# Performance work log

Measured on AMD Instinct MI355X. Metric: run time of the kernel, lower is better.

Reference implementation:

```python
import jax, jax.numpy as jnp
import numpy as np

N_NODES = 50000
N_EDGES = 400000
MUL_IN = 32      # input node irreps: 32x0e
MUL_OUT = 64     # target irreps: 64x0e+64x1o+64x2e+64x3o
DENOM = 8.0

# component-normalized real spherical harmonics, l = 1, 2, 3, on unit vectors
_S3, _S5, _S7, _S15, _S42, _S70, _S105 = (np.sqrt(v).astype(np.float32) for v in (3., 5., 7., 15., 42., 70., 105.))

def spherical_harmonics_123(vec):
    # vec: [E, 3]; normalize=True semantics
    r = jnp.linalg.norm(vec, axis=-1, keepdims=True)
    u = vec / jnp.maximum(r, 1e-12)
    x, y, z = u[..., 0], u[..., 1], u[..., 2]
    x2, y2, z2 = x * x, y * y, z * z
    sh1 = jnp.stack([_S3 * x, _S3 * y, _S3 * z], axis=-1)                      # [E, 3]
    sh2 = jnp.stack([
        _S15 * x * y,
        _S15 * y * z,
        0.5 * _S5 * (3.0 * z2 - 1.0),
        _S15 * x * z,
        0.5 * _S15 * (x2 - y2),
    ], axis=-1)                                                                # [E, 5]
    sh3 = jnp.stack([
        0.25 * _S70 * y * (3.0 * x2 - y2),
        _S105 * x * y * z,
        0.25 * _S42 * y * (5.0 * z2 - 1.0),
        0.5 * _S7 * z * (5.0 * z2 - 3.0),
        0.25 * _S42 * x * (5.0 * z2 - 1.0),
        0.5 * _S105 * z * (x2 - y2),
        0.25 * _S70 * x * (x2 - 3.0 * y2),
    ], axis=-1)                                                                # [E, 7]
    return sh1, sh2, sh3


def setup_inputs() -> dict:
    key = jax.random.key(0)
    ks = jax.random.split(key, 9)
    return {
        "positions": jax.random.normal(ks[0], (N_NODES, 3), jnp.float32),
        "node_feats": jax.random.normal(ks[1], (N_NODES, MUL_IN), jnp.float32),
        "W0": jax.random.normal(ks[2], (MUL_IN, MUL_OUT), jnp.float32),
        "W1": jax.random.normal(ks[3], (MUL_IN, MUL_OUT), jnp.float32),
        "W2": jax.random.normal(ks[4], (MUL_IN, MUL_OUT), jnp.float32),
        "W3": jax.random.normal(ks[5], (MUL_IN, MUL_OUT), jnp.float32),
        "Wsc": jax.random.normal(ks[6], (MUL_IN, MUL_OUT), jnp.float32),
        "senders": jax.random.randint(ks[7], (N_EDGES,), 0, N_NODES),
        "receivers": jax.random.randint(ks[8], (N_EDGES,), 0, N_NODES),
    }


def reference(positions, node_feats, W0, W1, W2, W3, Wsc, senders, receivers):
    E = senders.shape[0]
    # ---- update_edge_fn: gather senders, SH of edge vectors, 0e x l tensor product ----
    sf = node_feats[senders]                                      # [E, 32] (32x0e)
    rel = positions[receivers] - positions[senders]               # [E, 3]
    sh1, sh2, sh3 = spherical_harmonics_123(rel)
    # tensor product 32x0e (x) (1o+2e+3o): CG for 0e x l -> l is identity
    tp1 = (sf[:, :, None] * sh1[:, None, :]).reshape(E, -1)       # [E, 32*3]
    tp2 = (sf[:, :, None] * sh2[:, None, :]).reshape(E, -1)       # [E, 32*5]
    tp3 = (sf[:, :, None] * sh3[:, None, :]).reshape(E, -1)       # [E, 32*7]
    messages = jnp.concatenate([sf, tp1, tp2, tp3], axis=-1)      # [E, 512]: 32x0e+32x1o+32x2e+32x3o

    # ---- GraphNetwork aggregation: sum messages at receivers ----
    agg = jax.ops.segment_sum(messages, receivers, num_segments=N_NODES)  # [N, 512]
    nf = agg / DENOM

    # ---- update_node_fn: e3nn Linear per-l (path-normalized by 1/sqrt(fan_in)) ----
    scale = 1.0 / np.sqrt(MUL_IN).astype(np.float32)
    s = nf[:, :MUL_IN]                                            # [N, 32]
    v1 = nf[:, MUL_IN:MUL_IN * 4].reshape(-1, MUL_IN, 3)
    v2 = nf[:, MUL_IN * 4:MUL_IN * 9].reshape(-1, MUL_IN, 5)
    v3 = nf[:, MUL_IN * 9:].reshape(-1, MUL_IN, 7)

    out0 = (s @ W0) * scale                                       # [N, 64]
    out1 = jnp.einsum('nmi,mt->nti', v1, W1) * scale              # [N, 64, 3]
    out2 = jnp.einsum('nmi,mt->nti', v2, W2) * scale              # [N, 64, 5]
    out3 = jnp.einsum('nmi,mt->nti', v3, W3) * scale              # [N, 64, 7]

    # shortcut Linear from 32x0e (force_irreps_out: only the 0e block is nonzero)
    out0 = out0 + (node_feats @ Wsc) * scale

    N = node_feats.shape[0]
    return jnp.concatenate(
        [out0, out1.reshape(N, -1), out2.reshape(N, -1), out3.reshape(N, -1)], axis=-1
    )  # [N, 1024]
```

## Files before the change

### kernel.cpp

```cpp
#include <hip/hip_runtime.h>

#define NN 50000
#define NE 400000
#define SCAN_NB 196

__global__ void k_hist(const int* __restrict__ rcv, int* __restrict__ cnt){
  int e = blockIdx.x*256 + threadIdx.x;
  if (e < NE) atomicAdd(&cnt[rcv[e]], 1);
}

__global__ void k_scanA(const int* __restrict__ cnt, int* __restrict__ bsum){
  __shared__ int sh[256];
  int i = blockIdx.x*256 + threadIdx.x;
  int v = (i < NN) ? cnt[i] : 0;
  sh[threadIdx.x] = v; __syncthreads();
  for (int off=128; off>0; off>>=1){
    if (threadIdx.x < off) sh[threadIdx.x] += sh[threadIdx.x+off];
    __syncthreads();
  }
  if (threadIdx.x==0) bsum[blockIdx.x] = sh[0];
}

__global__ void k_scanB(int* __restrict__ bsum){
  __shared__ int sh[256];
  int t = threadIdx.x;
  int v = (t < SCAN_NB) ? bsum[t] : 0;
  sh[t] = v; __syncthreads();
  for (int off=1; off<256; off<<=1){
    int x = (t>=off)? sh[t-off] : 0;
    __syncthreads();
    sh[t] += x;
    __syncthreads();
  }
  if (t < SCAN_NB) bsum[t] = sh[t] - v;
}

__global__ void k_scanC(const int* __restrict__ cnt, const int* __restrict__ bsum,
                        int* __restrict__ offs, int* __restrict__ cursor){
  __shared__ int sh[256];
  int t = threadIdx.x;
  int i = blockIdx.x*256 + t;
  int v = (i < NN) ? cnt[i] : 0;
  sh[t] = v; __syncthreads();
  for (int off=1; off<256; off<<=1){
    int x = (t>=off)? sh[t-off] : 0;
    __syncthreads();
    sh[t] += x;
    __syncthreads();
  }
  int excl = sh[t] - v + bsum[blockIdx.x];
  if (i < NN){ offs[i] = excl; cursor[i] = excl; }
}

__global__ void k_scatter(const int* __restrict__ rcv, const int* __restrict__ snd,
                          int* __restrict__ cursor, int* __restrict__ csr_snd){
  int e = blockIdx.x*256 + threadIdx.x;
  if (e < NE){
    int p = atomicAdd(&cursor[rcv[e]], 1);
    csr_snd[p] = snd[e];
  }
}

__global__ void k_prepW(const float* __restrict__ W0, const float* __restrict__ W1,
                        const float* __restrict__ W2, const float* __restrict__ W3,
                        float4* __restrict__ Wp){
  int i = blockIdx.x*256 + threadIdx.x;
  if (i < 2048) Wp[i] = make_float4(W0[i], W1[i], W2[i], W3[i]);
}

__global__ __launch_bounds__(256) void k_main(
    const float* __restrict__ pos, const float* __restrict__ feat,
    const float4* __restrict__ Wp, const float* __restrict__ Wsc,
    const int* __restrict__ offs, const int* __restrict__ cnt,
    const int* __restrict__ csr_snd, float* __restrict__ out)
{
  __shared__ __align__(16) float smS[4][1024];

  const int tid = threadIdx.x, wv = tid>>6, lane = tid&63;
  const int ml = lane&31, hh = lane>>5;
  const int n = blockIdx.x*4 + wv;
  const float pnx=pos[n*3], pny=pos[n*3+1], pnz=pos[n*3+2];
  const int start = offs[n], deg = cnt[n];
  const int nch = (deg+63)>>6;

  float acc[8];
  #pragma unroll
  for (int j=0;j<8;++j) acc[j]=0.f;

  const float SC3=1.7320508f, SC5=2.236068f, SC7=2.6457513f, SC15=3.8729833f,
              SC42=6.4807407f, SC70=8.3666003f, SC105=10.246951f;

  for (int c=0; c<nch; ++c){
    const int base = c<<6;
    int cn = deg - base; cn = (cn>64)?64:cn;
    int sE = 0;
    if (lane < cn){
      sE = csr_snd[start+base+lane];
      float rx = pnx - pos[sE*3];
      float ry = pny - pos[sE*3+1];
      float rz = pnz - pos[sE*3+2];
      float r = sqrtf(rx*rx+ry*ry+rz*rz);
      float inv = 1.0f/fmaxf(r,1e-12f);
      float x=rx*inv, y=ry*inv, z=rz*inv;
      float x2=x*x, y2=y*y, z2=z*z;
      float s1=SC3*x, s2=SC3*y, s3=SC3*z;
      float s4=SC15*x*y, s5=SC15*y*z, s6=0.5f*SC5*(3.f*z2-1.f), s7=SC15*x*z;
      float s8=0.5f*SC15*(x2-y2);
      float s9 =0.25f*SC70*y*(3.f*x2-y2);
      float s10=SC105*x*y*z;
      float s11=0.25f*SC42*y*(5.f*z2-1.f);
      float s12=0.5f*SC7*z*(5.f*z2-3.f);
      float s13=0.25f*SC42*x*(5.f*z2-1.f);
      float s14=0.5f*SC105*z*(x2-y2);
      float s15=0.25f*SC70*x*(x2-3.f*y2);
      float4* wp = (float4*)&smS[wv][lane*16];
      wp[0] = make_float4(1.0f,s1,s2,s3);
      wp[1] = make_float4(s4,s5,s6,s7);
      wp[2] = make_float4(s8,s9,s10,s11);
      wp[3] = make_float4(s12,s13,s14,s15);
    }
    asm volatile("s_waitcnt lgkmcnt(0)" ::: "memory");
    #pragma unroll 8
    for (int it=0; it<cn; ++it){
      int s = __builtin_amdgcn_readlane(sE, it);
      float f = feat[(size_t)s*32 + ml];
      const float4* rp = (const float4*)&smS[wv][it*16 + hh*8];
      float4 q0=rp[0], q1=rp[1];
      acc[0]+=f*q0.x; acc[1]+=f*q0.y; acc[2]+=f*q0.z; acc[3]+=f*q0.w;
      acc[4]+=f*q1.x; acc[5]+=f*q1.y; acc[6]+=f*q1.z; acc[7]+=f*q1.w;
    }
    asm volatile("" ::: "memory");
  }

  {
    float4* ap = (float4*)&smS[wv][ml*16 + hh*8];
    ap[0] = make_float4(acc[0],acc[1],acc[2],acc[3]);
    ap[1] = make_float4(acc[4],acc[5],acc[6],acc[7]);
  }
  asm volatile("s_waitcnt lgkmcnt(0)" ::: "memory");

  float oa[16];
  #pragma unroll
  for (int k=0;k<16;++k) oa[k]=0.f;
  float osc = 0.f;
  const float4* f4 = (const float4*)(feat + (size_t)n*32);

  #pragma unroll 2
  for (int g=0; g<8; ++g){
    float4 fsv = f4[g];
    #pragma unroll
    for (int mm=0; mm<4; ++mm){
      const int m = g*4+mm;
      float4 wq = Wp[m*64 + lane];
      float  w4 = Wsc[m*64 + lane];
      const float4* Ap = (const float4*)&smS[wv][m*16];
      float4 a0=Ap[0], a1=Ap[1], a2=Ap[2], a3=Ap[3];
      const float fsm = (mm==0)?fsv.x:(mm==1)?fsv.y:(mm==2)?fsv.z:fsv.w;
      oa[0] += a0.x*wq.x;
      oa[1] += a0.y*wq.y; oa[2] += a0.z*wq.y; oa[3] += a0.w*wq.y;
      oa[4] += a1.x*wq.z; oa[5] += a1.y*wq.z; oa[6] += a1.z*wq.z;
      oa[7] += a1.w*wq.z; oa[8] += a2.x*wq.z;
      oa[9] += a2.y*wq.w; oa[10]+= a2.z*wq.w; oa[11]+= a2.w*wq.w;
      oa[12]+= a3.x*wq.w; oa[13]+= a3.y*wq.w; oa[14]+= a3.z*wq.w; oa[15]+= a3.w*wq.w;
      osc += fsm*w4;
    }
  }
  asm volatile("" ::: "memory");

  const float S = 0.17677669529663687f;
  const float S8 = S*0.125f;
  float* ol = &smS[wv][0];
  ol[lane] = oa[0]*S8 + osc*S;
  #pragma unroll
  for (int i=0;i<3;++i) ol[64  + lane*3 + i] = oa[1+i]*S8;
  #pragma unroll
  for (int i=0;i<5;++i) ol[256 + lane*5 + i] = oa[4+i]*S8;
  #pragma unroll
  for (int i=0;i<7;++i) ol[576 + lane*7 + i] = oa[9+i]*S8;
  asm volatile("s_waitcnt lgkmcnt(0)" ::: "memory");

  float4* o4 = (float4*)(out + (size_t)n*1024);
  const float4* s4 = (const float4*)&smS[wv][0];
  #pragma unroll
  for (int i=0;i<4;++i) o4[i*64 + lane] = s4[i*64 + lane];
}

extern "C" void kernel_launch(void* const* d_in, const int* in_sizes, int n_in,
                              void* d_out, int out_size, void* d_ws, size_t ws_size,
                              hipStream_t stream) {
  const float* pos  = (const float*)d_in[0];
  const float* feat = (const float*)d_in[1];
  const float* W0   = (const float*)d_in[2];
  const float* W1   = (const float*)d_in[3];
  const float* W2   = (const float*)d_in[4];
  const float* W3   = (const float*)d_in[5];
  const float* Wsc  = (const float*)d_in[6];
  const int*  snd   = (const int*)d_in[7];
  const int*  rcv   = (const int*)d_in[8];
  float* out = (float*)d_out;

  int* ws      = (int*)d_ws;
  int* cnt     = ws;
  int* offs    = ws + 50000;
  int* cursor  = ws + 100000;
  int* bsum    = ws + 150000;
  int* csr_snd = ws + 150272;
  float4* Wp   = (float4*)(ws + 550272);

  hipMemsetAsync(cnt, 0, NN*sizeof(int), stream);
  k_hist   <<<(NE+255)/256, 256, 0, stream>>>(rcv, cnt);
  k_scanA  <<<SCAN_NB, 256, 0, stream>>>(cnt, bsum);
  k_scanB  <<<1, 256, 0, stream>>>(bsum);
  k_scanC  <<<SCAN_NB, 256, 0, stream>>>(cnt, bsum, offs, cursor);
  k_scatter<<<(NE+255)/256, 256, 0, stream>>>(rcv, snd, cursor, csr_snd);
  k_prepW  <<<8, 256, 0, stream>>>(W0, W1, W2, W3, Wp);
  k_main   <<<12500, 256, 0, stream>>>(pos, feat, Wp, Wsc,
                                       offs, cnt, csr_snd, out);
}
```

Baseline: 396.3 us.

## Process two nodes per wavefront and broadcast aggregates via readlane

```diff
diff --git a/kernel.cpp b/kernel.cpp
--- a/kernel.cpp
+++ b/kernel.cpp
@@ -74,115 +74,123 @@
     const int* __restrict__ offs, const int* __restrict__ cnt,
     const int* __restrict__ csr_snd, float* __restrict__ out)
 {
-  __shared__ __align__(16) float smS[4][1024];
+  __shared__ __align__(16) float smS[4][1280];
 
   const int tid = threadIdx.x, wv = tid>>6, lane = tid&63;
   const int ml = lane&31, hh = lane>>5;
-  const int n = blockIdx.x*4 + wv;
-  const float pnx=pos[n*3], pny=pos[n*3+1], pnz=pos[n*3+2];
-  const int start = offs[n], deg = cnt[n];
-  const int nch = (deg+63)>>6;
-
-  float acc[8];
-  #pragma unroll
-  for (int j=0;j<8;++j) acc[j]=0.f;
+  const int nb = blockIdx.x*8 + wv*2;
 
   const float SC3=1.7320508f, SC5=2.236068f, SC7=2.6457513f, SC15=3.8729833f,
               SC42=6.4807407f, SC70=8.3666003f, SC105=10.246951f;
 
-  for (int c=0; c<nch; ++c){
-    const int base = c<<6;
-    int cn = deg - base; cn = (cn>64)?64:cn;
-    int sE = 0;
-    if (lane < cn){
-      sE = csr_snd[start+base+lane];
-      float rx = pnx - pos[sE*3];
-      float ry = pny - pos[sE*3+1];
-      float rz = pnz - pos[sE*3+2];
-      float r = sqrtf(rx*rx+ry*ry+rz*rz);
-      float inv = 1.0f/fmaxf(r,1e-12f);
-      float x=rx*inv, y=ry*inv, z=rz*inv;
-      float x2=x*x, y2=y*y, z2=z*z;
-      float s1=SC3*x, s2=SC3*y, s3=SC3*z;
-      float s4=SC15*x*y, s5=SC15*y*z, s6=0.5f*SC5*(3.f*z2-1.f), s7=SC15*x*z;
-      float s8=0.5f*SC15*(x2-y2);
-      float s9 =0.25f*SC70*y*(3.f*x2-y2);
-      float s10=SC105*x*y*z;
-      float s11=0.25f*SC42*y*(5.f*z2-1.f);
-      float s12=0.5f*SC7*z*(5.f*z2-3.f);
-      float s13=0.25f*SC42*x*(5.f*z2-1.f);
-      float s14=0.5f*SC105*z*(x2-y2);
-      float s15=0.25f*SC70*x*(x2-3.f*y2);
-      float4* wp = (float4*)&smS[wv][lane*16];
-      wp[0] = make_float4(1.0f,s1,s2,s3);
-      wp[1] = make_float4(s4,s5,s6,s7);
-      wp[2] = make_float4(s8,s9,s10,s11);
-      wp[3] = make_float4(s12,s13,s14,s15);
+  float acc[2][8];
+  #pragma unroll
+  for (int nn=0;nn<2;++nn)
+    #pragma unroll
+    for (int j=0;j<8;++j) acc[nn][j]=0.f;
+
+  #pragma unroll
+  for (int nn=0; nn<2; ++nn){
+    const int n = nb + nn;
+    const float pnx=pos[n*3], pny=pos[n*3+1], pnz=pos[n*3+2];
+    const int start = offs[n], deg = cnt[n];
+    const int nch = (deg+63)>>6;
+    for (int c=0; c<nch; ++c){
+      const int base = c<<6;
+      int cn = deg - base; cn = (cn>64)?64:cn;
+      int sE = 0;
+      if (lane < cn){
+        sE = csr_snd[start+base+lane];
+        float rx = pnx - pos[sE*3];
+        float ry = pny - pos[sE*3+1];
+        float rz = pnz - pos[sE*3+2];
+        float r = sqrtf(rx*rx+ry*ry+rz*rz);
+        float inv = 1.0f/fmaxf(r,1e-12f);
+        float x=rx*inv, y=ry*inv, z=rz*inv;
+        float x2=x*x, y2=y*y, z2=z*z;
+        float s1=SC3*x, s2=SC3*y, s3=SC3*z;
+        float s4=SC15*x*y, s5=SC15*y*z, s6=0.5f*SC5*(3.f*z2-1.f), s7=SC15*x*z;
+        float s8=0.5f*SC15*(x2-y2);
+        float s9 =0.25f*SC70*y*(3.f*x2-y2);
+        float s10=SC105*x*y*z;
+        float s11=0.25f*SC42*y*(5.f*z2-1.f);
+        float s12=0.5f*SC7*z*(5.f*z2-3.f);
+        float s13=0.25f*SC42*x*(5.f*z2-1.f);
+        float s14=0.5f*SC105*z*(x2-y2);
+        float s15=0.25f*SC70*x*(x2-3.f*y2);
+        float4* wp = (float4*)&smS[wv][lane*20];
+        wp[0] = make_float4(1.0f,s1,s2,s3);
+        wp[1] = make_float4(s4,s5,s6,s7);
+        wp[2] = make_float4(s8,s9,s10,s11);
+        wp[3] = make_float4(s12,s13,s14,s15);
+      }
+      asm volatile("s_waitcnt lgkmcnt(0)" ::: "memory");
+      #pragma unroll 8
+      for (int it=0; it<cn; ++it){
+        int s = __builtin_amdgcn_readlane(sE, it);
+        float f = feat[(size_t)s*32 + ml];
+        const float4* rp = (const float4*)&smS[wv][it*20 + hh*8];
+        float4 q0=rp[0], q1=rp[1];
+        acc[nn][0]+=f*q0.x; acc[nn][1]+=f*q0.y;
+        acc[nn][2]+=f*q0.z; acc[nn][3]+=f*q0.w;
+        acc[nn][4]+=f*q1.x; acc[nn][5]+=f*q1.y;
+        acc[nn][6]+=f*q1.z; acc[nn][7]+=f*q1.w;
+      }
+      asm volatile("" ::: "memory");
     }
-    asm volatile("s_waitcnt lgkmcnt(0)" ::: "memory");
-    #pragma unroll 8
-    for (int it=0; it<cn; ++it){
-      int s = __builtin_amdgcn_readlane(sE, it);
-      float f = feat[(size_t)s*32 + ml];
-      const float4* rp = (const float4*)&smS[wv][it*16 + hh*8];
-      float4 q0=rp[0], q1=rp[1];
-      acc[0]+=f*q0.x; acc[1]+=f*q0.y; acc[2]+=f*q0.z; acc[3]+=f*q0.w;
-      acc[4]+=f*q1.x; acc[5]+=f*q1.y; acc[6]+=f*q1.z; acc[7]+=f*q1.w;
+  }
+
+  const int n0 = __builtin_amdgcn_readfirstlane(nb);
+  const float* fn0 = feat + (size_t)n0*32;
+  const float* fn1 = fn0 + 32;
+
+  float oa[2][16];
+  #pragma unroll
+  for (int nn=0;nn<2;++nn)
+    #pragma unroll
+    for (int k=0;k<16;++k) oa[nn][k]=0.f;
+  float osc0=0.f, osc1=0.f;
+
+  #pragma unroll 4
+  for (int m=0; m<32; ++m){
+    float4 wq = Wp[m*64 + lane];
+    float  w4 = Wsc[m*64 + lane];
+    float f0 = fn0[m], f1 = fn1[m];
+    osc0 += f0*w4; osc1 += f1*w4;
+    #pragma unroll
+    for (int k=0;k<16;++k){
+      const int src = m + ((k>>3)<<5);
+      float a0 = __int_as_float(__builtin_amdgcn_readlane(
+                   __float_as_int(acc[0][k&7]), src));
+      float a1 = __int_as_float(__builtin_amdgcn_readlane(
+                   __float_as_int(acc[1][k&7]), src));
+      const float w = (k==0)?wq.x : (k<4)?wq.y : (k<9)?wq.z : wq.w;
+      oa[0][k] += a0*w;
+      oa[1][k] += a1*w;
     }
-    asm volatile("" ::: "memory");
-  }
-
-  {
-    float4* ap = (float4*)&smS[wv][ml*16 + hh*8];
-    ap[0] = make_float4(acc[0],acc[1],acc[2],acc[3]);
-    ap[1] = make_float4(acc[4],acc[5],acc[6],acc[7]);
-  }
-  asm volatile("s_waitcnt lgkmcnt(0)" ::: "memory");
-
-  float oa[16];
-  #pragma unroll
-  for (int k=0;k<16;++k) oa[k]=0.f;
-  float osc = 0.f;
-  const float4* f4 = (const float4*)(feat + (size_t)n*32);
-
-  #pragma unroll 2
-  for (int g=0; g<8; ++g){
-    float4 fsv = f4[g];
-    #pragma unroll
-    for (int mm=0; mm<4; ++mm){
-      const int m = g*4+mm;
-      float4 wq = Wp[m*64 + lane];
-      float  w4 = Wsc[m*64 + lane];
-      const float4* Ap = (const float4*)&smS[wv][m*16];
-      float4 a0=Ap[0], a1=Ap[1], a2=Ap[2], a3=Ap[3];
-      const float fsm = (mm==0)?fsv.x:(mm==1)?fsv.y:(mm==2)?fsv.z:fsv.w;
-      oa[0] += a0.x*wq.x;
-      oa[1] += a0.y*wq.y; oa[2] += a0.z*wq.y; oa[3] += a0.w*wq.y;
-      oa[4] += a1.x*wq.z; oa[5] += a1.y*wq.z; oa[6] += a1.z*wq.z;
-      oa[7] += a1.w*wq.z; oa[8] += a2.x*wq.z;
-      oa[9] += a2.y*wq.w; oa[10]+= a2.z*wq.w; oa[11]+= a2.w*wq.w;
-      oa[12]+= a3.x*wq.w; oa[13]+= a3.y*wq.w; oa[14]+= a3.z*wq.w; oa[15]+= a3.w*wq.w;
-      osc += fsm*w4;
-    }
-  }
-  asm volatile("" ::: "memory");
+  }
 
   const float S = 0.17677669529663687f;
   const float S8 = S*0.125f;
-  float* ol = &smS[wv][0];
-  ol[lane] = oa[0]*S8 + osc*S;
-  #pragma unroll
-  for (int i=0;i<3;++i) ol[64  + lane*3 + i] = oa[1+i]*S8;
-  #pragma unroll
-  for (int i=0;i<5;++i) ol[256 + lane*5 + i] = oa[4+i]*S8;
-  #pragma unroll
-  for (int i=0;i<7;++i) ol[576 + lane*7 + i] = oa[9+i]*S8;
-  asm volatile("s_waitcnt lgkmcnt(0)" ::: "memory");
-
-  float4* o4 = (float4*)(out + (size_t)n*1024);
-  const float4* s4 = (const float4*)&smS[wv][0];
-  #pragma unroll
-  for (int i=0;i<4;++i) o4[i*64 + lane] = s4[i*64 + lane];
+  #pragma unroll
+  for (int nn=0; nn<2; ++nn){
+    float* ol = &smS[wv][0];
+    const float osc = nn ? osc1 : osc0;
+    ol[lane] = oa[nn][0]*S8 + osc*S;
+    #pragma unroll
+    for (int i=0;i<3;++i) ol[64  + lane*3 + i] = oa[nn][1+i]*S8;
+    #pragma unroll
+    for (int i=0;i<5;++i) ol[256 + lane*5 + i] = oa[nn][4+i]*S8;
+    #pragma unroll
+    for (int i=0;i<7;++i) ol[576 + lane*7 + i] = oa[nn][9+i]*S8;
+    asm volatile("s_waitcnt lgkmcnt(0)" ::: "memory");
+
+    float4* o4 = (float4*)(out + (size_t)(n0+nn)*1024);
+    const float4* s4 = (const float4*)&smS[wv][0];
+    #pragma unroll
+    for (int i=0;i<4;++i) o4[i*64 + lane] = s4[i*64 + lane];
+    asm volatile("" ::: "memory");
+  }
 }
 
 extern "C" void kernel_launch(void* const* d_in, const int* in_sizes, int n_in,
@@ -214,6 +222,6 @@
   k_scanC  <<<SCAN_NB, 256, 0, stream>>>(cnt, bsum, offs, cursor);
   k_scatter<<<(NE+255)/256, 256, 0, stream>>>(rcv, snd, cursor, csr_snd);
   k_prepW  <<<8, 256, 0, stream>>>(W0, W1, W2, W3, Wp);
-  k_main   <<<12500, 256, 0, stream>>>(pos, feat, Wp, Wsc,
-                                       offs, cnt, csr_snd, out);
-}
+  k_main   <<<6250, 256, 0, stream>>>(pos, feat, Wp, Wsc,
+                                      offs, cnt, csr_snd, out);
+}
```

New measurement: 388.6 us. No clear change (-1.9%).
